# Kernel tuning notes

Hardware: AMD Instinct MI355X
Metric: run time of the kernel (lower is better)

Reference implementation:

```python
import jax, jax.numpy as jnp
import numpy as np
from jax import lax

B, H, L, DK = 8, 8, 1024, 64
BN_EPS = 1e-5


def _conv_bn_sm(x, w, b, g, beta, pad):
    # x: [B, H, L] (N=batch, C=h heads as channels, spatial=L)
    y = lax.conv_general_dilated(x, w, (1,), [(pad, pad)], dimension_numbers=("NCH", "OIH", "NCH"))
    y = y + b[None, :, None]
    # BatchNorm1d in training mode: batch stats over (N, L) per channel, biased var
    mu = jnp.mean(y, axis=(0, 2), keepdims=True)
    var = jnp.var(y, axis=(0, 2), keepdims=True)
    y = (y - mu) * (g[None, :, None] / jnp.sqrt(var + BN_EPS)) + beta[None, :, None]
    return jax.nn.softmax(y, axis=-1)


def setup_inputs() -> dict:
    key = jax.random.key(0)
    ks = jax.random.split(key, 20)
    n = lambda i, shape, s=1.0: jax.random.normal(ks[i], shape, dtype=jnp.float32) * s
    inp = {
        "Q": n(0, (B, H, L, DK)),
        "K": n(1, (B, H, L, DK)),
        "V": n(2, (B, H, L, DK)),
        "attn_mask": jnp.ones((1,), dtype=bool),
        # proj_q / proj_k: Linear(d_k, 1, bias=False) weight [1, d_k] -> stored as [d_k]
        "wq": n(3, (DK,), 0.1), "wk": n(4, (DK,), 0.1),
        # proj_back_q / proj_back_k: Linear(1, d_k, bias=False) weight [d_k, 1] -> [d_k]
        "wbq": n(5, (DK,), 0.1), "wbk": n(6, (DK,), 0.1),
        # Conv1d(h, h, f) weights [out=h, in=h, f] + bias [h]
        "cq3_w": n(7, (H, H, 3), 0.2), "cq3_b": n(8, (H,), 0.05),
        "cq9_w": n(9, (H, H, 9), 0.1), "cq9_b": n(10, (H,), 0.05),
        "ck3_w": n(11, (H, H, 3), 0.2), "ck3_b": n(12, (H,), 0.05),
        "ck9_w": n(13, (H, H, 9), 0.1), "ck9_b": n(14, (H,), 0.05),
        # BatchNorm1d affine params
        "bnq3_g": jnp.ones((H,), jnp.float32), "bnq3_b": jnp.zeros((H,), jnp.float32),
        "bnq9_g": jnp.ones((H,), jnp.float32), "bnq9_b": jnp.zeros((H,), jnp.float32),
        "bnk3_g": jnp.ones((H,), jnp.float32), "bnk3_b": jnp.zeros((H,), jnp.float32),
        "bnk9_g": jnp.ones((H,), jnp.float32), "bnk9_b": jnp.zeros((H,), jnp.float32),
    }
    return inp


def reference(Q, K, V, attn_mask, wq, wk, wbq, wbk,
              cq3_w, cq3_b, cq9_w, cq9_b, ck3_w, ck3_b, ck9_w, ck9_b,
              bnq3_g, bnq3_b, bnq9_g, bnq9_b, bnk3_g, bnk3_b, bnk9_g, bnk9_b):
    b, h, l, d_k = Q.shape
    l_k = K.shape[2]
    # proj to scalar per position, reshape to [b, h, l]
    Qp = jnp.einsum("bhld,d->bhl", Q, wq)
    Kp = jnp.einsum("bhld,d->bhl", K, wk)
    # multi-scale conv + BN(train) + softmax branches
    q0 = _conv_bn_sm(Qp, cq3_w, cq3_b, bnq3_g, bnq3_b, 1)
    q1 = _conv_bn_sm(Qp, cq9_w, cq9_b, bnq9_g, bnq9_b, 4)
    k0 = _conv_bn_sm(Kp, ck3_w, ck3_b, bnk3_g, bnk3_b, 1)
    k1 = _conv_bn_sm(Kp, ck9_w, ck9_b, bnk9_g, bnk9_b, 4)
    # faithful to torch: cat along dim 0 then C-order reshape to [b,h,l,2], max over last
    Qm = jnp.max(jnp.concatenate([q0, q1], axis=0).reshape(b, h, l, 2), axis=-1)
    Km = jnp.max(jnp.concatenate([k0, k1], axis=0).reshape(b, h, l_k, 2), axis=-1)
    # proj back 1 -> d_k (no bias): outer with weight vector
    Qn = Qm[..., None] * wbq  # [b,h,l,d_k]
    Kn = Km[..., None] * wbk  # [b,h,l_k,d_k]
    scores = jnp.einsum("bhqd,bhkd->bhqk", Qn, Kn) / jnp.sqrt(jnp.float32(d_k))
    attn = jax.nn.softmax(scores, axis=-1)
    context = jnp.einsum("bhqk,bhkd->bhqd", attn, V)
    return (context, attn)
```

## Files before the change

kernel.cpp:

```cpp
#include <hip/hip_runtime.h>

constexpr int SL = 1024;
constexpr int NBH = 64;

constexpr int QP_OFF = 0;
constexpr int KP_OFF = 65536;
constexpr int Y_OFF  = 131072;
constexpr int QM_OFF = 655360;
constexpr int KM_OFF = 720896;
constexpr int ST_OFF = 786432;
constexpr int C_OFF  = 786496;
constexpr int VT_OFF = 786560;

typedef __attribute__((ext_vector_type(8))) short short8;
typedef __attribute__((ext_vector_type(4))) float f32x4;

__device__ inline unsigned short f2bf(float x) {
    unsigned int u = __float_as_uint(x);
    unsigned int r = (u + 0x7fff + ((u >> 16) & 1)) >> 16;
    return (unsigned short)r;
}

__global__ __launch_bounds__(256) void k_projpack(
    const float* __restrict__ Q, const float* __restrict__ K,
    const float* __restrict__ V,
    const float* __restrict__ wq, const float* __restrict__ wk,
    const float* __restrict__ wbq, const float* __restrict__ wbk,
    float* __restrict__ ws)
{
    int b = blockIdx.x;
    int tid = threadIdx.x;
    if (b < 8192) {
        bool isQ = b < 4096;
        const float* src = isQ ? Q : K;
        const float* w   = isQ ? wq : wk;
        int row = (b - (isQ ? 0 : 4096)) * 16 + (tid >> 4);
        int l16 = tid & 15;
        float4 x  = ((const float4*)(src + row * 64))[l16];
        float4 w4 = ((const float4*)w)[l16];
        float v = x.x * w4.x + x.y * w4.y + x.z * w4.z + x.w * w4.w;
        #pragma unroll
        for (int m = 8; m; m >>= 1) v += __shfl_xor(v, m);
        if (l16 == 0) ws[(isQ ? QP_OFF : KP_OFF) + row] = v;
    } else if (b < 10240) {
        int t = (b - 8192) * 256 + tid;
        int lane = t & 63;
        int s    = (t >> 6) & 7;
        int dsub = (t >> 9) & 3;
        int chunk= (t >> 11) & 3;
        int bh   = t >> 13;
        const float* vb = V + bh * (SL * 64);
        int k0 = chunk * 256 + s * 32 + (lane >> 4) * 8;
        int d  = dsub * 16 + (lane & 15);
        unsigned short o[8];
        #pragma unroll
        for (int j = 0; j < 8; j++) o[j] = f2bf(vb[(k0 + j) * 64 + d]);
        unsigned short* vt = (unsigned short*)(ws + VT_OFF);
        *(short8*)(vt + (size_t)t * 8) = *(short8*)o;
    } else {
        if (tid < 64) {
            ws[ST_OFF + tid] = 0.f;
            float v = wbq[tid] * wbk[tid];
            #pragma unroll
            for (int m = 32; m; m >>= 1) v += __shfl_xor(v, m);
            if (tid == 0) ws[C_OFF] = v * 0.125f;
        }
    }
}

__global__ __launch_bounds__(256) void k_conv(
    float* __restrict__ ws,
    const float* __restrict__ w0, const float* __restrict__ b0,
    const float* __restrict__ w1, const float* __restrict__ b1,
    const float* __restrict__ w2, const float* __restrict__ b2,
    const float* __restrict__ w3, const float* __restrict__ b3)
{
    int branch = blockIdx.x >> 6;
    int n = (blockIdx.x >> 3) & 7;
    int seg = blockIdx.x & 7;
    int t0 = seg * 128;
    const float* wp = branch == 0 ? w0 : branch == 1 ? w1 : branch == 2 ? w2 : w3;
    const float* bp = branch == 0 ? b0 : branch == 1 ? b1 : branch == 2 ? b2 : b3;
    const int F = (branch & 1) ? 9 : 3;
    const int PAD = F >> 1;
    const float* x = ws + ((branch < 2) ? QP_OFF : KP_OFF) + n * 8 * SL;

    __shared__ float xl[8][136];
    __shared__ float wl[8 * 8 * 9];
    __shared__ float bl[8];
    int tid = threadIdx.x;
    for (int i = tid; i < 8 * 8 * F; i += 256) wl[i] = wp[i];
    if (tid < 8) bl[tid] = bp[tid];
    for (int i = tid; i < 8 * 136; i += 256) {
        int ci = i / 136; int tt = i - ci * 136;
        int ta = t0 + tt - 4;
        xl[ci][tt] = (ta >= 0 && ta < SL) ? x[ci * SL + ta] : 0.f;
    }
    __syncthreads();
    int c = tid >> 5, u = tid & 31;
    float s1 = 0.f, s2 = 0.f;
    float* yout = ws + Y_OFF + branch * (NBH * SL) + (n * 8 + c) * SL + t0;
    #pragma unroll
    for (int q = 0; q < 4; q++) {
        int tl = q * 32 + u;
        float acc = bl[c];
        for (int ci = 0; ci < 8; ci++) {
            const float* xr = &xl[ci][tl + 4 - PAD];
            const float* wr = &wl[(c * 8 + ci) * F];
            for (int f = 0; f < F; f++) acc += wr[f] * xr[f];
        }
        yout[tl] = acc;
        s1 += acc; s2 += acc * acc;
    }
    #pragma unroll
    for (int m = 16; m; m >>= 1) {
        s1 += __shfl_xor(s1, m);
        s2 += __shfl_xor(s2, m);
    }
    if (u == 0) {
        atomicAdd(&ws[ST_OFF + (branch * 8 + c) * 2],     s1);
        atomicAdd(&ws[ST_OFF + (branch * 8 + c) * 2 + 1], s2);
    }
}

__global__ __launch_bounds__(256) void k_bnmix(
    float* __restrict__ ws,
    const float* __restrict__ g0, const float* __restrict__ be0,
    const float* __restrict__ g1, const float* __restrict__ be1,
    const float* __restrict__ g2, const float* __restrict__ be2,
    const float* __restrict__ g3, const float* __restrict__ be3)
{
    int blk = blockIdx.x;
    int which = blk >> 6;
    int i = (blk >> 3) & 7, j = blk & 7;
    int n = 2 * i + (j >= 4 ? 1 : 0);
    int br = which * 2 + (n >= 8 ? 1 : 0);
    int row = n & 7;
    int tid = threadIdx.x;
    int half = tid >> 7;
    int u = tid & 127;
    int c = 2 * (j & 3) + half;
    const float* gp = br == 0 ? g0 : br == 1 ? g1 : br == 2 ? g2 : g3;
    const float* bp = br == 0 ? be0 : br == 1 ? be1 : br == 2 ? be2 : be3;
    float s1 = ws[ST_OFF + (br * 8 + c) * 2];
    float s2 = ws[ST_OFF + (br * 8 + c) * 2 + 1];
    float mu  = s1 * (1.f / 8192.f);
    float var = s2 * (1.f / 8192.f) - mu * mu;
    float sc = gp[c] * rsqrtf(var + 1e-5f);
    float sh = bp[c] - mu * sc;
    const float* y = ws + Y_OFF + br * (NBH * SL) + (row * 8 + c) * SL;
    float4 ya = ((const float4*)y)[u * 2];
    float4 yb = ((const float4*)y)[u * 2 + 1];
    float z[8] = { ya.x * sc + sh, ya.y * sc + sh, ya.z * sc + sh, ya.w * sc + sh,
                   yb.x * sc + sh, yb.y * sc + sh, yb.z * sc + sh, yb.w * sc + sh };
    float mx = z[0];
    #pragma unroll
    for (int q = 1; q < 8; q++) mx = fmaxf(mx, z[q]);
    __shared__ float r1[4], r2[4];
    #pragma unroll
    for (int m = 32; m; m >>= 1) mx = fmaxf(mx, __shfl_xor(mx, m));
    if ((tid & 63) == 0) r1[tid >> 6] = mx;
    __syncthreads();
    mx = half ? fmaxf(r1[2], r1[3]) : fmaxf(r1[0], r1[1]);
    float e[8];
    float s = 0.f;
    #pragma unroll
    for (int q = 0; q < 8; q++) { e[q] = __expf(z[q] - mx); s += e[q]; }
    #pragma unroll
    for (int m = 32; m; m >>= 1) s += __shfl_xor(s, m);
    if ((tid & 63) == 0) r2[tid >> 6] = s;
    __syncthreads();
    s = half ? (r2[2] + r2[3]) : (r2[0] + r2[1]);
    float inv = 1.f / s;
    float4 o = make_float4(fmaxf(e[0], e[1]) * inv, fmaxf(e[2], e[3]) * inv,
                           fmaxf(e[4], e[5]) * inv, fmaxf(e[6], e[7]) * inv);
    float* outp = ws + (which ? KM_OFF : QM_OFF) + i * 8192 + j * 1024 + half * 512;
    ((float4*)outp)[u] = o;
}

__global__ __launch_bounds__(256, 4) void k_attn(
    float* __restrict__ out, const float* __restrict__ ws)
{
    int p = blockIdx.x;
    int xcd = p & 7, idx = p >> 3;
    int bh = xcd + 8 * (idx >> 5);
    int qt2 = idx & 31;
    int tid = threadIdx.x;

    __shared__ __align__(16) float kml[1024];
    __shared__ float rmx[4], rmn[4];
    __shared__ float wsum0[4][16], wsum1[4][16];
    __shared__ float accred[4][16][64];

    const float* km = ws + KM_OFF + bh * SL;
    const float* qm = ws + QM_OFF + bh * SL + qt2 * 32;
    float c = ws[C_OFF];

    float lmax = -1e30f, lmin = 1e30f;
    #pragma unroll
    for (int i = 0; i < 4; i++) {
        float v = km[tid + 256 * i];
        kml[tid + 256 * i] = v;
        lmax = fmaxf(lmax, v); lmin = fminf(lmin, v);
    }
    #pragma unroll
    for (int m = 32; m; m >>= 1) {
        lmax = fmaxf(lmax, __shfl_xor(lmax, m));
        lmin = fminf(lmin, __shfl_xor(lmin, m));
    }
    if ((tid & 63) == 0) { rmx[tid >> 6] = lmax; rmn[tid >> 6] = lmin; }
    __syncthreads();

    int w = tid >> 6, lane = tid & 63;
    int m16 = lane & 15, kg = lane >> 4;
    float kmax = fmaxf(fmaxf(rmx[0], rmx[1]), fmaxf(rmx[2], rmx[3]));
    float kmin = fminf(fminf(rmn[0], rmn[1]), fminf(rmn[2], rmn[3]));
    float a0 = c * qm[m16];
    float a1 = c * qm[16 + m16];
    float mm0 = (a0 > 0.f) ? a0 * kmax : a0 * kmin;
    float mm1 = (a1 > 0.f) ? a1 * kmax : a1 * kmin;

    float rs0 = 0.f, rs1 = 0.f;
    #pragma unroll
    for (int s = 0; s < 8; s++) {
        const float4* kp = (const float4*)(kml + w * 256 + s * 32 + kg * 8);
        float4 ka = kp[0], kb = kp[1];
        rs0 += __expf(a0 * ka.x - mm0); rs1 += __expf(a1 * ka.x - mm1);
        rs0 += __expf(a0 * ka.y - mm0); rs1 += __expf(a1 * ka.y - mm1);
        rs0 += __expf(a0 * ka.z - mm0); rs1 += __expf(a1 * ka.z - mm1);
        rs0 += __expf(a0 * ka.w - mm0); rs1 += __expf(a1 * ka.w - mm1);
        rs0 += __expf(a0 * kb.x - mm0); rs1 += __expf(a1 * kb.x - mm1);
        rs0 += __expf(a0 * kb.y - mm0); rs1 += __expf(a1 * kb.y - mm1);
        rs0 += __expf(a0 * kb.z - mm0); rs1 += __expf(a1 * kb.z - mm1);
        rs0 += __expf(a0 * kb.w - mm0); rs1 += __expf(a1 * kb.w - mm1);
    }
    rs0 += __shfl_xor(rs0, 16); rs0 += __shfl_xor(rs0, 32);
    rs1 += __shfl_xor(rs1, 16); rs1 += __shfl_xor(rs1, 32);
    if (lane < 16) { wsum0[w][lane] = rs0; wsum1[w][lane] = rs1; }
    __syncthreads();
    float rr0 = 1.f / (wsum0[0][m16] + wsum0[1][m16] + wsum0[2][m16] + wsum0[3][m16]);
    float rr1 = 1.f / (wsum1[0][m16] + wsum1[1][m16] + wsum1[2][m16] + wsum1[3][m16]);

    int rA = lane >> 3;
    int k4 = (lane & 7) * 4;
    float aA0 = __shfl(a0, rA),     aB0 = __shfl(a0, rA + 8);
    float mA0 = __shfl(mm0, rA),    mB0 = __shfl(mm0, rA + 8);
    float rA0 = __shfl(rr0, rA),    rB0 = __shfl(rr0, rA + 8);
    float aA1 = __shfl(a1, rA),     aB1 = __shfl(a1, rA + 8);
    float mA1 = __shfl(mm1, rA),    mB1 = __shfl(mm1, rA + 8);
    float rA1 = __shfl(rr1, rA),    rB1 = __shfl(rr1, rA + 8);

    float* attn0 = out + 4194304 + ((size_t)(bh * SL + qt2 * 32)) * SL + w * 256 + k4;
    float* attnA0 = attn0 + (size_t)rA * SL;
    float* attnB0 = attn0 + (size_t)(rA + 8) * SL;
    float* attnA1 = attn0 + (size_t)(rA + 16) * SL;
    float* attnB1 = attn0 + (size_t)(rA + 24) * SL;
    const short8* vt8 = (const short8*)((const unsigned short*)(ws + VT_OFF))
                        + (size_t)bh * 8192 + w * 2048;

    f32x4 p0a = {0,0,0,0}, p0b = {0,0,0,0}, p0c = {0,0,0,0}, p0d = {0,0,0,0};
    f32x4 p1a = {0,0,0,0}, p1b = {0,0,0,0}, p1c = {0,0,0,0}, p1d = {0,0,0,0};

    #pragma unroll
    for (int s = 0; s < 8; s++) {
        int k0 = w * 256 + s * 32 + kg * 8;
        const float4* kp = (const float4*)(kml + k0);
        float4 ka = kp[0], kb = kp[1];
        const short8* bbase = vt8 + s * 64 + lane;
        short8 b0 = bbase[0 * 512];
        short8 b1 = bbase[1 * 512];
        short8 b2 = bbase[2 * 512];
        short8 b3 = bbase[3 * 512];

        float4 kv = *(const float4*)(kml + w * 256 + s * 32 + k4);
        {
            float4 oA = make_float4(__expf(aA0 * kv.x - mA0) * rA0,
                                    __expf(aA0 * kv.y - mA0) * rA0,
                                    __expf(aA0 * kv.z - mA0) * rA0,
                                    __expf(aA0 * kv.w - mA0) * rA0);
            float4 oB = make_float4(__expf(aB0 * kv.x - mB0) * rB0,
                                    __expf(aB0 * kv.y - mB0) * rB0,
                                    __expf(aB0 * kv.z - mB0) * rB0,
                                    __expf(aB0 * kv.w - mB0) * rB0);
            *(float4*)(attnA0 + s * 32) = oA;
            *(float4*)(attnB0 + s * 32) = oB;
            float4 oC = make_float4(__expf(aA1 * kv.x - mA1) * rA1,
                                    __expf(aA1 * kv.y - mA1) * rA1,
                                    __expf(aA1 * kv.z - mA1) * rA1,
                                    __expf(aA1 * kv.w - mA1) * rA1);
            float4 oD = make_float4(__expf(aB1 * kv.x - mB1) * rB1,
                                    __expf(aB1 * kv.y - mB1) * rB1,
                                    __expf(aB1 * kv.z - mB1) * rB1,
                                    __expf(aB1 * kv.w - mB1) * rB1);
            *(float4*)(attnA1 + s * 32) = oC;
            *(float4*)(attnB1 + s * 32) = oD;
        }

        {
            unsigned short af[8];
            af[0] = f2bf(__expf(a0 * ka.x - mm0) * rr0);
            af[1] = f2bf(__expf(a0 * ka.y - mm0) * rr0);
            af[2] = f2bf(__expf(a0 * ka.z - mm0) * rr0);
            af[3] = f2bf(__expf(a0 * ka.w - mm0) * rr0);
            af[4] = f2bf(__expf(a0 * kb.x - mm0) * rr0);
            af[5] = f2bf(__expf(a0 * kb.y - mm0) * rr0);
            af[6] = f2bf(__expf(a0 * kb.z - mm0) * rr0);
            af[7] = f2bf(__expf(a0 * kb.w - mm0) * rr0);
            short8 av = *(short8*)af;
            p0a = __builtin_amdgcn_mfma_f32_16x16x32_bf16(av, b0, p0a, 0, 0, 0);
            p0b = __builtin_amdgcn_mfma_f32_16x16x32_bf16(av, b1, p0b, 0, 0, 0);
            p0c = __builtin_amdgcn_mfma_f32_16x16x32_bf16(av, b2, p0c, 0, 0, 0);
            p0d = __builtin_amdgcn_mfma_f32_16x16x32_bf16(av, b3, p0d, 0, 0, 0);
        }
        {
            unsigned short af[8];
            af[0] = f2bf(__expf(a1 * ka.x - mm1) * rr1);
            af[1] = f2bf(__expf(a1 * ka.y - mm1) * rr1);
            af[2] = f2bf(__expf(a1 * ka.z - mm1) * rr1);
            af[3] = f2bf(__expf(a1 * ka.w - mm1) * rr1);
            af[4] = f2bf(__expf(a1 * kb.x - mm1) * rr1);
            af[5] = f2bf(__expf(a1 * kb.y - mm1) * rr1);
            af[6] = f2bf(__expf(a1 * kb.z - mm1) * rr1);
            af[7] = f2bf(__expf(a1 * kb.w - mm1) * rr1);
            short8 av = *(short8*)af;
            p1a = __builtin_amdgcn_mfma_f32_16x16x32_bf16(av, b0, p1a, 0, 0, 0);
            p1b = __builtin_amdgcn_mfma_f32_16x16x32_bf16(av, b1, p1b, 0, 0, 0);
            p1c = __builtin_amdgcn_mfma_f32_16x16x32_bf16(av, b2, p1c, 0, 0, 0);
            p1d = __builtin_amdgcn_mfma_f32_16x16x32_bf16(av, b3, p1d, 0, 0, 0);
        }
    }

    #pragma unroll
    for (int reg = 0; reg < 4; reg++) {
        int r = kg * 4 + reg;
        accred[w][r][ 0 + m16] = p0a[reg];
        accred[w][r][16 + m16] = p0b[reg];
        accred[w][r][32 + m16] = p0c[reg];
        accred[w][r][48 + m16] = p0d[reg];
    }
    __syncthreads();
    {
        int r  = tid >> 4;
        int d0 = (tid & 15) * 4;
        float4 s0 = *(const float4*)&accred[0][r][d0];
        float4 s1 = *(const float4*)&accred[1][r][d0];
        float4 s2 = *(const float4*)&accred[2][r][d0];
        float4 s3 = *(const float4*)&accred[3][r][d0];
        float4 o = make_float4(s0.x + s1.x + s2.x + s3.x,
                               s0.y + s1.y + s2.y + s3.y,
                               s0.z + s1.z + s2.z + s3.z,
                               s0.w + s1.w + s2.w + s3.w);
        float* ctx = out + ((size_t)(bh * SL + qt2 * 32 + r)) * 64 + d0;
        *(float4*)ctx = o;
    }
    __syncthreads();
    #pragma unroll
    for (int reg = 0; reg < 4; reg++) {
        int r = kg * 4 + reg;
        accred[w][r][ 0 + m16] = p1a[reg];
        accred[w][r][16 + m16] = p1b[reg];
        accred[w][r][32 + m16] = p1c[reg];
        accred[w][r][48 + m16] = p1d[reg];
    }
    __syncthreads();
    {
        int r  = tid >> 4;
        int d0 = (tid & 15) * 4;
        float4 s0 = *(const float4*)&accred[0][r][d0];
        float4 s1 = *(const float4*)&accred[1][r][d0];
        float4 s2 = *(const float4*)&accred[2][r][d0];
        float4 s3 = *(const float4*)&accred[3][r][d0];
        float4 o = make_float4(s0.x + s1.x + s2.x + s3.x,
                               s0.y + s1.y + s2.y + s3.y,
                               s0.z + s1.z + s2.z + s3.z,
                               s0.w + s1.w + s2.w + s3.w);
        float* ctx = out + ((size_t)(bh * SL + qt2 * 32 + 16 + r)) * 64 + d0;
        *(float4*)ctx = o;
    }
}

extern "C" void kernel_launch(void* const* d_in, const int* in_sizes, int n_in,
                              void* d_out, int out_size, void* d_ws, size_t ws_size,
                              hipStream_t stream)
{
    const float* Q      = (const float*)d_in[0];
    const float* K      = (const float*)d_in[1];
    const float* V      = (const float*)d_in[2];
    const float* wq     = (const float*)d_in[4];
    const float* wk     = (const float*)d_in[5];
    const float* wbq    = (const float*)d_in[6];
    const float* wbk    = (const float*)d_in[7];
    const float* cq3_w  = (const float*)d_in[8];
    const float* cq3_b  = (const float*)d_in[9];
    const float* cq9_w  = (const float*)d_in[10];
    const float* cq9_b  = (const float*)d_in[11];
    const float* ck3_w  = (const float*)d_in[12];
    const float* ck3_b  = (const float*)d_in[13];
    const float* ck9_w  = (const float*)d_in[14];
    const float* ck9_b  = (const float*)d_in[15];
    const float* bnq3_g = (const float*)d_in[16];
    const float* bnq3_b = (const float*)d_in[17];
    const float* bnq9_g = (const float*)d_in[18];
    const float* bnq9_b = (const float*)d_in[19];
    const float* bnk3_g = (const float*)d_in[20];
    const float* bnk3_b = (const float*)d_in[21];
    const float* bnk9_g = (const float*)d_in[22];
    const float* bnk9_b = (const float*)d_in[23];
    float* out = (float*)d_out;
    float* ws  = (float*)d_ws;

    k_projpack<<<10241, 256, 0, stream>>>(Q, K, V, wq, wk, wbq, wbk, ws);
    k_conv<<<256, 256, 0, stream>>>(ws, cq3_w, cq3_b, cq9_w, cq9_b,
                                    ck3_w, ck3_b, ck9_w, ck9_b);
    k_bnmix<<<128, 256, 0, stream>>>(ws, bnq3_g, bnq3_b, bnq9_g, bnq9_b,
                                     bnk3_g, bnk3_b, bnk9_g, bnk9_b);
    k_attn<<<2048, 256, 0, stream>>>(out, ws);
}
```

Measured before the change: 411.8 us.

## Split attention-probability writes into a separate streaming kernel

Moves the writing of the full attention matrix out of the MFMA context kernel into a new kernel, k_attnw. The context kernel now stores only per-row max and reciprocal-sum statistics to workspace. The new kernel recomputes exp values and writes each row with fully coalesced float4 stores. The aim is to decouple the 256 MB of strided attn stores from the MFMA loop and shrink its register pressure, at the cost of an extra launch and recomputing the exponentials.

```diff
diff --git a/kernel.cpp b/kernel.cpp
--- a/kernel.cpp
+++ b/kernel.cpp
@@ -11,6 +11,8 @@
 constexpr int ST_OFF = 786432;
 constexpr int C_OFF  = 786496;
 constexpr int VT_OFF = 786560;
+constexpr int MQ_OFF = 2883712;
+constexpr int RQ_OFF = 2949248;
 
 typedef __attribute__((ext_vector_type(8))) short short8;
 typedef __attribute__((ext_vector_type(4))) float f32x4;
@@ -179,7 +181,7 @@
 }
 
 __global__ __launch_bounds__(256, 4) void k_attn(
-    float* __restrict__ out, const float* __restrict__ ws)
+    float* __restrict__ out, float* __restrict__ ws)
 {
     int p = blockIdx.x;
     int xcd = p & 7, idx = p >> 3;
@@ -241,20 +243,14 @@
     float rr0 = 1.f / (wsum0[0][m16] + wsum0[1][m16] + wsum0[2][m16] + wsum0[3][m16]);
     float rr1 = 1.f / (wsum1[0][m16] + wsum1[1][m16] + wsum1[2][m16] + wsum1[3][m16]);
 
-    int rA = lane >> 3;
-    int k4 = (lane & 7) * 4;
-    float aA0 = __shfl(a0, rA),     aB0 = __shfl(a0, rA + 8);
-    float mA0 = __shfl(mm0, rA),    mB0 = __shfl(mm0, rA + 8);
-    float rA0 = __shfl(rr0, rA),    rB0 = __shfl(rr0, rA + 8);
-    float aA1 = __shfl(a1, rA),     aB1 = __shfl(a1, rA + 8);
-    float mA1 = __shfl(mm1, rA),    mB1 = __shfl(mm1, rA + 8);
-    float rA1 = __shfl(rr1, rA),    rB1 = __shfl(rr1, rA + 8);
-
-    float* attn0 = out + 4194304 + ((size_t)(bh * SL + qt2 * 32)) * SL + w * 256 + k4;
-    float* attnA0 = attn0 + (size_t)rA * SL;
-    float* attnB0 = attn0 + (size_t)(rA + 8) * SL;
-    float* attnA1 = attn0 + (size_t)(rA + 16) * SL;
-    float* attnB1 = attn0 + (size_t)(rA + 24) * SL;
+    if (w == 0 && lane < 16) {
+        int rb = bh * SL + qt2 * 32;
+        ws[MQ_OFF + rb + lane]      = mm0;
+        ws[MQ_OFF + rb + 16 + lane] = mm1;
+        ws[RQ_OFF + rb + lane]      = rr0;
+        ws[RQ_OFF + rb + 16 + lane] = rr1;
+    }
+
     const short8* vt8 = (const short8*)((const unsigned short*)(ws + VT_OFF))
                         + (size_t)bh * 8192 + w * 2048;
 
@@ -271,31 +267,6 @@
         short8 b1 = bbase[1 * 512];
         short8 b2 = bbase[2 * 512];
         short8 b3 = bbase[3 * 512];
-
-        float4 kv = *(const float4*)(kml + w * 256 + s * 32 + k4);
-        {
-            float4 oA = make_float4(__expf(aA0 * kv.x - mA0) * rA0,
-                                    __expf(aA0 * kv.y - mA0) * rA0,
-                                    __expf(aA0 * kv.z - mA0) * rA0,
-                                    __expf(aA0 * kv.w - mA0) * rA0);
-            float4 oB = make_float4(__expf(aB0 * kv.x - mB0) * rB0,
-                                    __expf(aB0 * kv.y - mB0) * rB0,
-                                    __expf(aB0 * kv.z - mB0) * rB0,
-                                    __expf(aB0 * kv.w - mB0) * rB0);
-            *(float4*)(attnA0 + s * 32) = oA;
-            *(float4*)(attnB0 + s * 32) = oB;
-            float4 oC = make_float4(__expf(aA1 * kv.x - mA1) * rA1,
-                                    __expf(aA1 * kv.y - mA1) * rA1,
-                                    __expf(aA1 * kv.z - mA1) * rA1,
-                                    __expf(aA1 * kv.w - mA1) * rA1);
-            float4 oD = make_float4(__expf(aB1 * kv.x - mB1) * rB1,
-                                    __expf(aB1 * kv.y - mB1) * rB1,
-                                    __expf(aB1 * kv.z - mB1) * rB1,
-                                    __expf(aB1 * kv.w - mB1) * rB1);
-            *(float4*)(attnA1 + s * 32) = oC;
-            *(float4*)(attnB1 + s * 32) = oD;
-        }
-
         {
             unsigned short af[8];
             af[0] = f2bf(__expf(a0 * ka.x - mm0) * rr0);
@@ -379,6 +350,43 @@
     }
 }
 
+__global__ __launch_bounds__(256, 8) void k_attnw(
+    float* __restrict__ out, const float* __restrict__ ws)
+{
+    int p = blockIdx.x;
+    int xcd = p & 7, idx = p >> 3;
+    int bh = xcd + 8 * (idx >> 4);
+    int qc = idx & 15;
+    int tid = threadIdx.x;
+
+    __shared__ __align__(16) float kml[1024];
+    __shared__ float aql[64], mql[64], rql[64];
+
+    const float* km = ws + KM_OFF + bh * SL;
+    #pragma unroll
+    for (int i = 0; i < 4; i++) kml[tid + 256 * i] = km[tid + 256 * i];
+    int rowbase = bh * SL + qc * 64;
+    if (tid < 64) {
+        float c = ws[C_OFF];
+        aql[tid] = c * ws[QM_OFF + rowbase + tid];
+        mql[tid] = ws[MQ_OFF + rowbase + tid];
+        rql[tid] = ws[RQ_OFF + rowbase + tid];
+    }
+    __syncthreads();
+
+    float4 kv = ((const float4*)kml)[tid];
+    float* attn = out + 4194304 + (size_t)rowbase * SL + tid * 4;
+    #pragma unroll 4
+    for (int r = 0; r < 64; ++r) {
+        float a = aql[r], mm = mql[r], rr = rql[r];
+        float4 o = make_float4(__expf(a * kv.x - mm) * rr,
+                               __expf(a * kv.y - mm) * rr,
+                               __expf(a * kv.z - mm) * rr,
+                               __expf(a * kv.w - mm) * rr);
+        *(float4*)(attn + (size_t)r * SL) = o;
+    }
+}
+
 extern "C" void kernel_launch(void* const* d_in, const int* in_sizes, int n_in,
                               void* d_out, int out_size, void* d_ws, size_t ws_size,
                               hipStream_t stream)
@@ -415,4 +423,5 @@
     k_bnmix<<<128, 256, 0, stream>>>(ws, bnq3_g, bnq3_b, bnq9_g, bnq9_b,
                                      bnk3_g, bnk3_b, bnk9_g, bnk9_b);
     k_attn<<<2048, 256, 0, stream>>>(out, ws);
-}
+    k_attnw<<<1024, 256, 0, stream>>>(out, ws);
+}
```

New measurement: 412.8 us. No clear change (+0.3%).
